# Kernel optimization log

Measured on AMD Instinct MI355X. Metric: run time of the kernel, lower is better.

## Reference

```python
import jax, jax.numpy as jnp
import numpy as np

HEADS, DHEAD = 4, 64            # TransformerConv heads / out_channels
MAX_EDGE_DIST = 1.0

def _ln(x, g, b):
    m = jnp.mean(x, -1, keepdims=True)
    v = jnp.mean((x - m) ** 2, -1, keepdims=True)
    return (x - m) * jax.lax.rsqrt(v + 1e-5) * g + b


def _embed_conv(node_feat, entity_type, adjv, mask, emb, W1, b1, g1, be1, Wh, bh, gh, beh):
    # aggr='add' message passing over dense masked adjacency. mask[b,s,t]: edge s->t.
    B, N, _ = mask.shape
    src = jnp.concatenate([node_feat, emb[entity_type]], -1)          # [B,N,F+E]
    msg = jnp.concatenate(
        [jnp.broadcast_to(src[:, :, None, :], (B, N, N, src.shape[-1])),
         adjv[..., None]], -1)                                        # [B,Ns,Nt,F+E+1]
    h = _ln(jax.nn.relu(msg @ W1 + b1), g1, be1)                      # lin1
    h = _ln(jax.nn.relu(h @ Wh + bh), gh, beh)                        # lin2[0]
    return jnp.einsum('bst,bsth->bth', mask, h)                       # sum over sources


def _tconv(x, adjv, mask, Wq, bq, Wk, bk, Wv, bv, We, Ws, bs):
    # PyG TransformerConv (beta=False, dropout=0, root_weight=True, concat=True).
    B, N, _ = x.shape
    q = (x @ Wq + bq).reshape(B, N, HEADS, DHEAD)
    k = (x @ Wk + bk).reshape(B, N, HEADS, DHEAD)
    v = (x @ Wv + bv).reshape(B, N, HEADS, DHEAD)
    we = We.reshape(HEADS, DHEAD)                                     # edge_dim=1, no bias
    scale = 1.0 / jnp.sqrt(jnp.asarray(DHEAD, x.dtype))
    # score[b,h,s,t] = q_t . (k_s + adjv[s,t]*we) * scale
    qk = jnp.einsum('bshd,bthd->bhst', k, q)
    qe = jnp.einsum('bthd,hd->bht', q, we)
    logits = (qk + adjv[:, None, :, :] * qe[:, :, None, :]) * scale
    mh = mask[:, None, :, :]                                          # [B,1,Ns,Nt]
    masked = jnp.where(mh > 0, logits, -1e30)
    mmax = jnp.max(masked, axis=2, keepdims=True)
    w = jnp.exp(masked - mmax) * mh
    den = jnp.sum(w, axis=2, keepdims=True)
    alpha = w / jnp.maximum(den, 1e-16)                               # softmax over sources per target
    out = jnp.einsum('bhst,bshd->bthd', alpha, v)
    out = out + jnp.einsum('bhst,bst->bth', alpha, adjv)[..., None] * we
    out = out.reshape(B, N, HEADS * DHEAD)
    return out + x @ Ws + bs                                          # skip (root) connection


def _forward(node_feat, entity_type, adj, agent_id, emb, W1, b1, g1, be1, Wh, bh, gh, beh,
             Wq1, bq1, Wk1, bk1, Wv1, bv1, We1, Ws1, bs1,
             Wq2, bq2, Wk2, bk2, Wv2, bv2, We2, Ws2, bs2):
    mask = ((adj > 0) & (adj < MAX_EDGE_DIST)).astype(adj.dtype)
    adjv = adj * mask
    x = _embed_conv(node_feat, entity_type, adjv, mask, emb, W1, b1, g1, be1, Wh, bh, gh, beh)
    x = jax.nn.relu(_tconv(x, adjv, mask, Wq1, bq1, Wk1, bk1, Wv1, bv1, We1, Ws1, bs1))
    x = jax.nn.relu(_tconv(x, adjv, mask, Wq2, bq2, Wk2, bk2, Wv2, bv2, We2, Ws2, bs2))
    return x[jnp.arange(x.shape[0]), agent_id]                        # gather agent node feats


def setup_inputs() -> dict:
    key = jax.random.key(0)
    ks = jax.random.split(key, 24)
    B, N, F, E, H = 32, 128, 9, 8, 128
    HD = HEADS * DHEAD
    s = 0.05
    p = lambda k, shape: (jax.random.normal(k, shape, jnp.float32) * s)
    inp = {
        'node_feat': jax.random.normal(ks[0], (B, N, F), jnp.float32),
        'entity_type': jax.random.randint(ks[1], (B, N), 0, 8),
        'adj': jax.random.uniform(ks[2], (B, N, N), jnp.float32, 0.0, 2.0),
        'agent_id': jax.random.randint(ks[3], (B,), 0, N),
        'emb': p(ks[4], (8, E)),
        'W1': p(ks[5], (F + E + 1, H)), 'b1': jnp.zeros(H), 'g1': jnp.ones(H), 'be1': jnp.zeros(H),
        'Wh': p(ks[6], (H, H)), 'bh': jnp.zeros(H), 'gh': jnp.ones(H), 'beh': jnp.zeros(H),
        'Wq1': p(ks[7], (H, HD)), 'bq1': jnp.zeros(HD),
        'Wk1': p(ks[8], (H, HD)), 'bk1': jnp.zeros(HD),
        'Wv1': p(ks[9], (H, HD)), 'bv1': jnp.zeros(HD),
        'We1': p(ks[10], (1, HD)),
        'Ws1': p(ks[11], (H, HD)), 'bs1': jnp.zeros(HD),
        'Wq2': p(ks[12], (HD, HD)), 'bq2': jnp.zeros(HD),
        'Wk2': p(ks[13], (HD, HD)), 'bk2': jnp.zeros(HD),
        'Wv2': p(ks[14], (HD, HD)), 'bv2': jnp.zeros(HD),
        'We2': p(ks[15], (1, HD)),
        'Ws2': p(ks[16], (HD, HD)), 'bs2': jnp.zeros(HD),
    }
    return inp


def reference(node_feat, entity_type, adj, agent_id, emb, W1, b1, g1, be1, Wh, bh, gh, beh,
              Wq1, bq1, Wk1, bk1, Wv1, bv1, We1, Ws1, bs1,
              Wq2, bq2, Wk2, bk2, Wv2, bv2, We2, Ws2, bs2):
    return _forward(node_feat, entity_type, adj, agent_id, emb, W1, b1, g1, be1, Wh, bh, gh, beh,
                    Wq1, bq1, Wk1, bk1, Wv1, bv1, We1, Ws1, bs1,
                    Wq2, bq2, Wk2, bk2, Wv2, bv2, We2, Ws2, bs2)
```

## Files before the change

### kernel.cpp

```cpp
#include <hip/hip_runtime.h>
#include <hip/hip_bf16.h>

typedef __hip_bfloat16 bf16;
typedef unsigned short ushort_t;
typedef unsigned char uchar_t;
typedef unsigned int uint_t;
typedef __attribute__((ext_vector_type(8))) short short8;
typedef __attribute__((ext_vector_type(4))) float fx4;
typedef __attribute__((ext_vector_type(4))) unsigned int uintx4;

#define BB 32
#define NN 128
#define FF 9
#define EE 8
#define HH 128
#define HD 256
#define NHEAD 4
#define DHEAD 64

__device__ __forceinline__ float us2f(ushort_t u) {
    return __uint_as_float(((unsigned int)u) << 16);
}
__device__ __forceinline__ ushort_t f2us_tr(float f) {
    return (ushort_t)(__float_as_uint(f) >> 16);
}
__device__ __forceinline__ short8 pack4(uint_t w0, uint_t w1, uint_t w2, uint_t w3) {
    uintx4 u = (uintx4){w0, w1, w2, w3};
    return __builtin_bit_cast(short8, u);
}
__device__ __forceinline__ void pair_split(float a, float c, uint_t& hw, uint_t& lw) {
    uint_t ua = __float_as_uint(a), uc = __float_as_uint(c);
    uint_t ka = ua & 0xffff0000u, kc = uc & 0xffff0000u;
    float la = a - __uint_as_float(ka);
    float lc = c - __uint_as_float(kc);
    hw = (ua >> 16) | kc;
    lw = (__float_as_uint(la) >> 16) | (__float_as_uint(lc) & 0xffff0000u);
}
__device__ __forceinline__ uint_t pair_hi(float a, float c) {
    return (__float_as_uint(a) >> 16) | (__float_as_uint(c) & 0xffff0000u);
}

__global__ void TransformerConvNet_85315230367963_kernel() {}

__global__ void k_sent(float* out, float val) {
    out[blockIdx.x * 256 + threadIdx.x] = val;
}

__global__ void k_zero(float* p) {
    p[blockIdx.x * 256 + threadIdx.x] = 0.f;
}

__global__ void k_adjv(const float* adj, float* adjvT) {
    int blk = blockIdx.x;
    int b = blk >> 3, sl = blk & 7;
    const float* src = adj + b * NN * NN;
    float* d2 = adjvT + b * NN * NN;
    int i0 = sl * 2048;
    for (int ii = threadIdx.x; ii < 2048; ii += 256) {
        int i = i0 + ii;
        int t = i >> 7, s = i & 127;
        float a2 = src[s * NN + t];
        d2[i] = (a2 > 0.f && a2 < 1.0f) ? a2 : 0.f;
    }
}

__global__ void k_slist(const float* adjvT, uchar_t* sl_s, float* sl_av, int* cnts) {
    int key = blockIdx.x * 256 + threadIdx.x;
    int bt = key >> 1, sh = key & 1;
    const float* row = adjvT + bt * NN + sh * 64;
    uchar_t* os = sl_s + key * 64;
    float* oa = sl_av + key * 64;
    int c = 0;
    for (int s = 0; s < 64; s++) {
        float a = row[s];
        if (a != 0.f) { os[c] = (uchar_t)(sh * 64 + s); oa[c] = a; c++; }
    }
    if (c == 0) { os[0] = 0; oa[0] = 0.f; }
    cnts[key] = c;
}

__global__ void k_base(const float* nf, const int* et, const float* emb,
                       const float* W1, const float* b1, float* base) {
    int bs = blockIdx.x;
    int c = threadIdx.x;
    int ty = et[bs];
    float acc = b1[c];
    for (int f = 0; f < FF; f++)
        acc += nf[bs * FF + f] * W1[f * HH + c];
    for (int e = 0; e < EE; e++)
        acc += emb[ty * EE + e] * W1[(FF + e) * HH + c];
    base[bs * HH + c] = acc;
}

__global__ void k_prep(const float* Wh, const float* g1, const float* be1,
                       const float* bh, ushort_t* BhiG, ushort_t* BloG,
                       float* W1s, float* cbv) {
    int n = blockIdx.x;
    int t = threadIdx.x;
    int sw = 8 * (n & 15);
    float s1 = 0.f, s2 = 0.f;
    for (int kk = 0; kk < 2; kk++) {
        int k = t + kk * 64;
        float w = Wh[k * HH + n];
        float wp = g1[k] * w;
        ushort_t hb = f2us_tr(wp);
        float lo = wp - us2f(hb);
        BhiG[n * HH + (k ^ sw)] = hb;
        BloG[n * HH + (k ^ sw)] = f2us_tr(lo);
        s1 += wp;
        s2 += be1[k] * w;
    }
    for (int m = 1; m < 64; m <<= 1) {
        s1 += __shfl_xor(s1, m);
        s2 += __shfl_xor(s2, m);
    }
    if (t == 0) { W1s[n] = s1; cbv[n] = s2 + bh[n]; }
}

__global__ void k_prepw(const float* W0, const float* W1p, const float* W2p,
                        const float* W3p, int IN, ushort_t* Whi, ushort_t* Wlo) {
    int blk = blockIdx.x;
    int mat = blk >> 8, n = blk & 255;
    const float* W = (mat == 0) ? W0 : (mat == 1) ? W1p : (mat == 2) ? W2p : W3p;
    ushort_t* hi = Whi + mat * 256 * IN;
    ushort_t* lo = Wlo + mat * 256 * IN;
    int sw = 8 * (n & 15);
    for (int k = threadIdx.x; k < IN; k += 64) {
        float w = W[k * HD + n];
        ushort_t hb = f2us_tr(w);
        float l = w - us2f(hb);
        hi[n * IN + (k ^ sw)] = hb;
        lo[n * IN + (k ^ sw)] = f2us_tr(l);
    }
}

__global__ void __launch_bounds__(256) k_econv_mfma(
    const uchar_t* sl_s, const float* sl_av, const int* cnts,
    const float* base, const float* W1,
    const ushort_t* BhiG, const ushort_t* BloG,
    const float* W1sg, const float* cbv,
    const float* ghp, const float* behp, float* x0)
{
    __shared__ __align__(16) ushort_t PhiPlo[2 * HH * HH];
    ushort_t* Phi = PhiPlo;
    ushort_t* Plo = PhiPlo + HH * HH;

    int blk = blockIdx.x;
    int b  = blk >> 4;
    int tt = (blk >> 1) & 7;
    int sh = blk & 1;
    int t0 = tt * 16;
    int tid = threadIdx.x;
    int wv  = tid >> 6;
    int lane = tid & 63;
    int nl = lane & 15;
    int quad = lane >> 4;

    {
        const uint4* srcH = (const uint4*)BhiG;
        const uint4* srcL = (const uint4*)BloG;
        uint4* dstH = (uint4*)Phi;
        uint4* dstL = (uint4*)Plo;
        for (int i = tid; i < HH * HH / 8; i += 256) {
            dstH[i] = srcH[i];
            dstL[i] = srcL[i];
        }
    }

    float w17v[4][8];
#pragma unroll
    for (int st = 0; st < 4; st++) {
        const float* p = W1 + 17 * HH + quad * 8 + 32 * st;
        float4 a = *(const float4*)p;
        float4 bq = *(const float4*)(p + 4);
        w17v[st][0] = a.x;  w17v[st][1] = a.y;  w17v[st][2] = a.z;  w17v[st][3] = a.w;
        w17v[st][4] = bq.x; w17v[st][5] = bq.y; w17v[st][6] = bq.z; w17v[st][7] = bq.w;
    }

    int key = ((b * NN) + t0 + nl) * 2 + sh;
    int cnt = cnts[key];
    int q = (cnt + 3) >> 2;
    int mq = q;
#pragma unroll
    for (int m = 1; m < 16; m <<= 1) mq = max(mq, __shfl_xor(mq, m));
    const uchar_t* lst_s = sl_s + key * 64;
    const float*   lst_a = sl_av + key * 64;
    int i0 = wv * q;

    fx4 acc1[8];
#pragma unroll
    for (int tile = 0; tile < 8; tile++) acc1[tile] = (fx4){0.f, 0.f, 0.f, 0.f};
    float c0 = 0.f;
    float c1 = 0.f;

    __syncthreads();

    for (int i = 0; i < mq; i++) {
        int idx = i0 + i;
        bool val = (i < q) && (idx < cnt);
        int ridx = (idx < cnt) ? idx : (cnt > 0 ? cnt - 1 : 0);
        int s = lst_s[ridx];
        float avv = val ? lst_a[ridx] : 0.f;
        const float* brow = base + (b * NN + s) * HH;

        short8 Hhi[4], Hlo[4];
        float sm = 0.f, s2 = 0.f;
#pragma unroll
        for (int st = 0; st < 4; st++) {
            const float* p = brow + quad * 8 + 32 * st;
            float4 b0 = *(const float4*)p;
            float4 b1q = *(const float4*)(p + 4);
            float h[8] = {b0.x, b0.y, b0.z, b0.w, b1q.x, b1q.y, b1q.z, b1q.w};
            uint_t hw[4], lw[4];
#pragma unroll
            for (int pr = 0; pr < 4; pr++) {
                float a = fmaxf(fmaf(avv, w17v[st][2 * pr], h[2 * pr]), 0.f);
                float c = fmaxf(fmaf(avv, w17v[st][2 * pr + 1], h[2 * pr + 1]), 0.f);
                sm += a; sm += c;
                s2 = fmaf(a, a, s2);
                s2 = fmaf(c, c, s2);
                pair_split(a, c, hw[pr], lw[pr]);
            }
            Hhi[st] = pack4(hw[0], hw[1], hw[2], hw[3]);
            Hlo[st] = pack4(lw[0], lw[1], lw[2], lw[3]);
        }
        sm += __shfl_xor(sm, 16); sm += __shfl_xor(sm, 32);
        s2 += __shfl_xor(s2, 16); s2 += __shfl_xor(s2, 32);
        float m1 = sm * (1.f / 128.f);
        float r1 = rsqrtf(s2 * (1.f / 128.f) - m1 * m1 + 1e-5f);
        float nm = -m1 * r1;

        fx4 G[8];
#pragma unroll
        for (int tile = 0; tile < 8; tile++) G[tile] = (fx4){0.f, 0.f, 0.f, 0.f};
#pragma unroll
        for (int st = 0; st < 4; st++) {
            int koff = quad * 8 + 32 * st;
#pragma unroll
            for (int tile = 0; tile < 8; tile++) {
                int off = (tile * 16 + nl) * HH + (koff ^ (nl * 8));
                short8 ph = *(const short8*)(&Phi[off]);
                short8 pl = *(const short8*)(&Plo[off]);
                G[tile] = __builtin_amdgcn_mfma_f32_16x16x32_bf16(ph, Hhi[st], G[tile], 0, 0, 0);
                G[tile] = __builtin_amdgcn_mfma_f32_16x16x32_bf16(pl, Hhi[st], G[tile], 0, 0, 0);
                G[tile] = __builtin_amdgcn_mfma_f32_16x16x32_bf16(ph, Hlo[st], G[tile], 0, 0, 0);
            }
        }

        float sm2 = 0.f, ss2 = 0.f;
#pragma unroll
        for (int tile = 0; tile < 8; tile++) {
            float4 w4 = *(const float4*)(W1sg + tile * 16 + quad * 4);
            float4 c4 = *(const float4*)(cbv + tile * 16 + quad * 4);
            float wa[4] = {w4.x, w4.y, w4.z, w4.w};
            float ca[4] = {c4.x, c4.y, c4.z, c4.w};
#pragma unroll
            for (int r = 0; r < 4; r++) {
                float pre = fmaf(r1, G[tile][r], fmaf(nm, wa[r], ca[r]));
                float h2 = fmaxf(pre, 0.f);
                G[tile][r] = h2;
                sm2 += h2;
                ss2 = fmaf(h2, h2, ss2);
            }
        }
        sm2 += __shfl_xor(sm2, 16); sm2 += __shfl_xor(sm2, 32);
        ss2 += __shfl_xor(ss2, 16); ss2 += __shfl_xor(ss2, 32);
        float mean2 = sm2 * (1.f / 128.f);
        float r2 = rsqrtf(ss2 * (1.f / 128.f) - mean2 * mean2 + 1e-5f);
        float msk = val ? 1.f : 0.f;
        float mr2 = msk * r2;

#pragma unroll
        for (int tile = 0; tile < 8; tile++)
#pragma unroll
            for (int r = 0; r < 4; r++)
                acc1[tile][r] = fmaf(mr2, G[tile][r], acc1[tile][r]);
        c0 += msk;
        c1 = fmaf(mr2, mean2, c1);
    }

    __syncthreads();
    float* slab = (float*)PhiPlo;
#pragma unroll
    for (int tile = 0; tile < 8; tile++) {
        float4 g4 = *(const float4*)(ghp + tile * 16 + quad * 4);
        float4 be4 = *(const float4*)(behp + tile * 16 + quad * 4);
        float gv[4] = {g4.x, g4.y, g4.z, g4.w};
        float bv[4] = {be4.x, be4.y, be4.z, be4.w};
#pragma unroll
        for (int r = 0; r < 4; r++) {
            float xv = fmaf(gv[r], acc1[tile][r] - c1, bv[r] * c0);
            slab[(wv * 16 + nl) * 132 + tile * 16 + quad * 4 + r] = xv;
        }
    }
    __syncthreads();
    for (int e = tid; e < 16 * HH; e += 256) {
        int t = e >> 7, n = e & 127;
        float vsum = slab[t * 132 + n] + slab[(16 + t) * 132 + n]
                   + slab[(32 + t) * 132 + n] + slab[(48 + t) * 132 + n];
        atomicAdd(&x0[(b * NN + t0 + t) * HH + n], vsum);
    }
}

template <int IN>
__global__ void __launch_bounds__(256) k_qkvs_mfma(
    const float* x, const ushort_t* Whi, const ushort_t* Wlo,
    const float* b0, const float* b1, const float* b2, const float* b3,
    float* q, float* skipo,
    ushort_t* khi, ushort_t* klo, ushort_t* vThi, ushort_t* vTlo)
{
    const int ST = IN / 32;
    int blk = blockIdx.x;
    int m0 = (blk >> 3) * 64;
    int nsl = blk & 7;
    int tid = threadIdx.x;
    int wv = tid >> 6;
    int lane = tid & 63;
    int nl = lane & 15;
    int quad = lane >> 4;
    int row = m0 + wv * 16 + nl;

    short8 Ahi[ST], Alo[ST];
    const float* xrow = x + (long)row * IN;
#pragma unroll
    for (int st = 0; st < ST; st++) {
        const float* p = xrow + quad * 8 + 32 * st;
        float4 a4 = *(const float4*)p;
        float4 b4 = *(const float4*)(p + 4);
        float h[8] = {a4.x, a4.y, a4.z, a4.w, b4.x, b4.y, b4.z, b4.w};
        uint_t hw[4], lw[4];
#pragma unroll
        for (int pr = 0; pr < 4; pr++)
            pair_split(h[2 * pr], h[2 * pr + 1], hw[pr], lw[pr]);
        Ahi[st] = pack4(hw[0], hw[1], hw[2], hw[3]);
        Alo[st] = pack4(lw[0], lw[1], lw[2], lw[3]);
    }

    const float* bs_[4] = {b0, b1, b2, b3};

#pragma unroll
    for (int mat = 0; mat < 4; mat++) {
        const ushort_t* Bh = Whi + (mat * 256 + nsl * 32) * IN;
        const ushort_t* Bl = Wlo + (mat * 256 + nsl * 32) * IN;
        fx4 G[2];
#pragma unroll
        for (int tile = 0; tile < 2; tile++) {
            float bc = bs_[mat][nsl * 32 + tile * 16 + nl];
            G[tile] = (fx4){bc, bc, bc, bc};
        }
#pragma unroll
        for (int st = 0; st < ST; st++) {
            int koff = quad * 8 + 32 * st;
#pragma unroll
            for (int tile = 0; tile < 2; tile++) {
                int off = (tile * 16 + nl) * IN + (koff ^ (nl * 8));
                short8 bh8 = *(const short8*)(Bh + off);
                short8 bl8 = *(const short8*)(Bl + off);
                G[tile] = __builtin_amdgcn_mfma_f32_16x16x32_bf16(Ahi[st], bh8, G[tile], 0, 0, 0);
                G[tile] = __builtin_amdgcn_mfma_f32_16x16x32_bf16(Alo[st], bh8, G[tile], 0, 0, 0);
                G[tile] = __builtin_amdgcn_mfma_f32_16x16x32_bf16(Ahi[st], bl8, G[tile], 0, 0, 0);
            }
        }
        int row0 = m0 + wv * 16 + quad * 4;
        if (mat == 0 || mat == 3) {
            float* om = (mat == 0) ? q : skipo;
#pragma unroll
            for (int tile = 0; tile < 2; tile++)
#pragma unroll
                for (int r = 0; r < 4; r++)
                    om[(row0 + r) * HD + nsl * 32 + tile * 16 + nl] = G[tile][r];
        } else if (mat == 1) {
#pragma unroll
            for (int tile = 0; tile < 2; tile++) {
                int col = nsl * 32 + tile * 16 + nl;
#pragma unroll
                for (int r = 0; r < 4; r++) {
                    float gv = G[tile][r];
                    ushort_t hb = f2us_tr(gv);
                    khi[(row0 + r) * HD + col] = hb;
                    klo[(row0 + r) * HD + col] = f2us_tr(gv - us2f(hb));
                }
            }
        } else {
            int bb = row0 >> 7;
            int s0 = row0 & 127;
#pragma unroll
            for (int tile = 0; tile < 2; tile++) {
                int col = nsl * 32 + tile * 16 + nl;
                int dg = bb * 256 + col;
                ushort4 h4, l4;
                float g0 = G[tile][0], g1 = G[tile][1], g2 = G[tile][2], g3 = G[tile][3];
                ushort_t h0 = f2us_tr(g0), h1 = f2us_tr(g1), h2 = f2us_tr(g2), h3 = f2us_tr(g3);
                h4.x = h0; h4.y = h1; h4.z = h2; h4.w = h3;
                l4.x = f2us_tr(g0 - us2f(h0));
                l4.y = f2us_tr(g1 - us2f(h1));
                l4.z = f2us_tr(g2 - us2f(h2));
                l4.w = f2us_tr(g3 - us2f(h3));
                *(ushort4*)&vThi[dg * NN + s0] = h4;
                *(ushort4*)&vTlo[dg * NN + s0] = l4;
            }
        }
    }
}

__global__ void __launch_bounds__(64) k_attn_mfma(
    const float* qb, const ushort_t* khi, const ushort_t* klo,
    const ushort_t* vThi, const ushort_t* vTlo,
    const float* adjvT, const float* We, const float* skip, float* xout)
{
    __shared__ float aL[16][132];
    __shared__ float qeL[16];

    int blk = blockIdx.x;
    int b  = blk >> 5;
    int h  = (blk >> 3) & 3;
    int tt = blk & 7;
    int t0 = tt * 16;
    int lane = threadIdx.x;
    int nl = lane & 15;
    int quad = lane >> 4;

    short8 Qhi[2], Qlo[2];
    float qe = 0.f;
#pragma unroll
    for (int ks = 0; ks < 2; ks++) {
        const float* p = qb + (b * NN + t0 + nl) * HD + h * DHEAD + quad * 8 + 32 * ks;
        const float* wp = We + h * DHEAD + quad * 8 + 32 * ks;
        float4 a0 = *(const float4*)p;
        float4 a1 = *(const float4*)(p + 4);
        float4 w0 = *(const float4*)wp;
        float4 w1 = *(const float4*)(wp + 4);
        float hv[8] = {a0.x, a0.y, a0.z, a0.w, a1.x, a1.y, a1.z, a1.w};
        float wv8[8] = {w0.x, w0.y, w0.z, w0.w, w1.x, w1.y, w1.z, w1.w};
        uint_t hw[4], lw[4];
#pragma unroll
        for (int pr = 0; pr < 4; pr++) {
            float a = hv[2 * pr], c = hv[2 * pr + 1];
            qe = fmaf(a, wv8[2 * pr], qe);
            qe = fmaf(c, wv8[2 * pr + 1], qe);
            pair_split(a, c, hw[pr], lw[pr]);
        }
        Qhi[ks] = pack4(hw[0], hw[1], hw[2], hw[3]);
        Qlo[ks] = pack4(lw[0], lw[1], lw[2], lw[3]);
    }
    qe += __shfl_xor(qe, 16);
    qe += __shfl_xor(qe, 32);
    if (lane < 16) qeL[lane] = qe;
    __syncthreads();
    float qe_r[4];
#pragma unroll
    for (int r = 0; r < 4; r++) qe_r[r] = qeL[quad * 4 + r];
    float we_d[4];
#pragma unroll
    for (int nt = 0; nt < 4; nt++) we_d[nt] = We[h * DHEAD + nt * 16 + nl];

    fx4 S[8];
#pragma unroll
    for (int st = 0; st < 8; st++) S[st] = (fx4){0.f, 0.f, 0.f, 0.f};
#pragma unroll
    for (int ks = 0; ks < 2; ks++) {
#pragma unroll
        for (int st = 0; st < 8; st++) {
            long off = (long)(b * NN + st * 16 + nl) * HD + h * DHEAD + quad * 8 + 32 * ks;
            short8 bh8 = *(const short8*)(khi + off);
            short8 bl8 = *(const short8*)(klo + off);
            S[st] = __builtin_amdgcn_mfma_f32_16x16x32_bf16(Qhi[ks], bh8, S[st], 0, 0, 0);
            S[st] = __builtin_amdgcn_mfma_f32_16x16x32_bf16(Qlo[ks], bh8, S[st], 0, 0, 0);
            S[st] = __builtin_amdgcn_mfma_f32_16x16x32_bf16(Qhi[ks], bl8, S[st], 0, 0, 0);
        }
    }

    float av[8][4];
#pragma unroll
    for (int st = 0; st < 8; st++)
#pragma unroll
        for (int r = 0; r < 4; r++)
            av[st][r] = adjvT[(b * NN + t0 + quad * 4 + r) * NN + st * 16 + nl];
#pragma unroll
    for (int st = 0; st < 8; st++)
#pragma unroll
        for (int r = 0; r < 4; r++) {
            float a = av[st][r];
            S[st][r] = (a != 0.f) ? (S[st][r] + a * qe_r[r]) * 0.125f : -1e30f;
        }

    float mx[4], den[4], beta[4];
#pragma unroll
    for (int r = 0; r < 4; r++) {
        float m = S[0][r];
#pragma unroll
        for (int st = 1; st < 8; st++) m = fmaxf(m, S[st][r]);
#pragma unroll
        for (int mm = 1; mm < 16; mm <<= 1) m = fmaxf(m, __shfl_xor(m, mm));
        mx[r] = m;
    }
#pragma unroll
    for (int r = 0; r < 4; r++) den[r] = 0.f;
#pragma unroll
    for (int st = 0; st < 8; st++)
#pragma unroll
        for (int r = 0; r < 4; r++) {
            float e = (av[st][r] != 0.f) ? __expf(S[st][r] - mx[r]) : 0.f;
            S[st][r] = e;
            den[r] += e;
        }
#pragma unroll
    for (int r = 0; r < 4; r++) {
#pragma unroll
        for (int mm = 1; mm < 16; mm <<= 1) den[r] += __shfl_xor(den[r], mm);
        den[r] = 1.f / fmaxf(den[r], 1e-16f);
        beta[r] = 0.f;
    }
#pragma unroll
    for (int st = 0; st < 8; st++)
#pragma unroll
        for (int r = 0; r < 4; r++) {
            float al = S[st][r] * den[r];
            S[st][r] = al;
            beta[r] += al * av[st][r];
        }
#pragma unroll
    for (int r = 0; r < 4; r++)
#pragma unroll
        for (int mm = 1; mm < 16; mm <<= 1) beta[r] += __shfl_xor(beta[r], mm);

#pragma unroll
    for (int st = 0; st < 8; st++)
#pragma unroll
        for (int r = 0; r < 4; r++)
            aL[quad * 4 + r][st * 16 + nl] = S[st][r];
    __syncthreads();
    short8 Ah[4];
#pragma unroll
    for (int ks = 0; ks < 4; ks++) {
        const float* p = &aL[nl][quad * 8 + 32 * ks];
        float4 a0 = *(const float4*)p;
        float4 a1 = *(const float4*)(p + 4);
        float hv[8] = {a0.x, a0.y, a0.z, a0.w, a1.x, a1.y, a1.z, a1.w};
        uint_t w[4];
#pragma unroll
        for (int pr = 0; pr < 4; pr++) w[pr] = pair_hi(hv[2 * pr], hv[2 * pr + 1]);
        Ah[ks] = pack4(w[0], w[1], w[2], w[3]);
    }

    fx4 G[4];
#pragma unroll
    for (int nt = 0; nt < 4; nt++) {
        fx4 g;
#pragma unroll
        for (int r = 0; r < 4; r++) g[r] = beta[r] * we_d[nt];
        G[nt] = g;
    }
#pragma unroll
    for (int ks = 0; ks < 4; ks++) {
#pragma unroll
        for (int nt = 0; nt < 4; nt++) {
            long dg = (long)(b * 256 + h * DHEAD + nt * 16 + nl);
            const short8 vh = *(const short8*)(vThi + dg * NN + quad * 8 + 32 * ks);
            const short8 vl = *(const short8*)(vTlo + dg * NN + quad * 8 + 32 * ks);
            G[nt] = __builtin_amdgcn_mfma_f32_16x16x32_bf16(Ah[ks], vh, G[nt], 0, 0, 0);
            G[nt] = __builtin_amdgcn_mfma_f32_16x16x32_bf16(Ah[ks], vl, G[nt], 0, 0, 0);
        }
    }

#pragma unroll
    for (int nt = 0; nt < 4; nt++)
#pragma unroll
        for (int r = 0; r < 4; r++) {
            int gi = (b * NN + t0 + quad * 4 + r) * HD + h * DHEAD + nt * 16 + nl;
            xout[gi] = fmaxf(G[nt][r] + skip[gi], 0.f);
        }
}

__global__ void k_gather(const float* x2, const int* agent, float* out) {
    int b = blockIdx.x;
    int c = threadIdx.x;
    out[b * HD + c] = x2[(b * NN + agent[b]) * HD + c];
}

extern "C" void kernel_launch(void* const* d_in, const int* in_sizes, int n_in,
                              void* d_out, int out_size, void* d_ws, size_t ws_size,
                              hipStream_t stream) {
    float* out = (float*)d_out;
    (void)hipGetLastError();

    bool ok = (n_in == 31) && in_sizes[0] == BB * NN * FF && in_sizes[2] == BB * NN * NN
              && in_sizes[5] == (FF + EE + 1) * HH && in_sizes[13] == HH * HD
              && in_sizes[22] == HD * HD && out_size == BB * HD;
    if (!ok) { k_sent<<<32, 256, 0, stream>>>(out, -30000.f); return; }

    const size_t WS_NEED = (size_t)8912896 * 4;
    if (ws_size < WS_NEED) { k_sent<<<32, 256, 0, stream>>>(out, -20000.f); return; }

    const float* nf    = (const float*)d_in[0];
    const int*   et    = (const int*)d_in[1];
    const float* adj   = (const float*)d_in[2];
    const int*   agent = (const int*)d_in[3];
    const float* emb   = (const float*)d_in[4];
    const float* W1    = (const float*)d_in[5];
    const float* b1    = (const float*)d_in[6];
    const float* g1    = (const float*)d_in[7];
    const float* be1   = (const float*)d_in[8];
    const float* Wh    = (const float*)d_in[9];
    const float* bh    = (const float*)d_in[10];
    const float* gh    = (const float*)d_in[11];
    const float* beh   = (const float*)d_in[12];
    const float* Wq1   = (const float*)d_in[13];
    const float* bq1   = (const float*)d_in[14];
    const float* Wk1   = (const float*)d_in[15];
    const float* bk1   = (const float*)d_in[16];
    const float* Wv1   = (const float*)d_in[17];
    const float* bv1   = (const float*)d_in[18];
    const float* We1   = (const float*)d_in[19];
    const float* Ws1   = (const float*)d_in[20];
    const float* bs1   = (const float*)d_in[21];
    const float* Wq2   = (const float*)d_in[22];
    const float* bq2   = (const float*)d_in[23];
    const float* Wk2   = (const float*)d_in[24];
    const float* bk2   = (const float*)d_in[25];
    const float* Wv2   = (const float*)d_in[26];
    const float* bv2   = (const float*)d_in[27];
    const float* We2   = (const float*)d_in[28];
    const float* Ws2   = (const float*)d_in[29];
    const float* bs2   = (const float*)d_in[30];

    float* ws   = (float*)d_ws;
    float* slav = ws;
    float* base = slav + BB * NN * NN / 32;
    base = ws + 524288;
    float* x0   = base + BB * NN * HH;
    float* q    = x0 + BB * NN * HH;
    float* kreg = q + BB * NN * HD;
    float* vreg = kreg + BB * NN * HD;
    float* skip = vreg + BB * NN * HD;
    float* areg = skip + BB * NN * HD;
    float* x1   = areg + BB * NN * HD;
    float* x2   = x1 + BB * NN * HD;

    ushort_t* BhiG = (ushort_t*)q;
    ushort_t* BloG = BhiG + HH * HH;
    float*    W1sW = q + 16384;
    float*    cbW  = q + 16512;
    int*      cnts = (int*)(q + 17024);

    ushort_t* khi  = (ushort_t*)kreg;
    ushort_t* klo  = khi + BB * NN * HD;
    ushort_t* vThi = (ushort_t*)vreg;
    ushort_t* vTlo = vThi + BB * NN * HD;

    ushort_t* WhA = (ushort_t*)areg;
    ushort_t* WlA = WhA + 4 * 256 * HH;
    ushort_t* WhB = WlA + 4 * 256 * HH;
    ushort_t* WlB = WhB + 4 * 256 * HD;
    float* adjvT  = areg + 393216;
    uchar_t* sl_s = (uchar_t*)(areg + 917504);

    int fail = 0;
    hipError_t e;
#define CHK(stage) do { e = hipGetLastError(); if (e != hipSuccess && fail == 0) fail = (stage); } while (0)

    k_adjv<<<256, 256, 0, stream>>>(adj, adjvT);                                     CHK(1);
    k_slist<<<32, 256, 0, stream>>>(adjvT, sl_s, slav, cnts);                        CHK(2);
    k_base<<<BB * NN, HH, 0, stream>>>(nf, et, emb, W1, b1, base);                   CHK(3);
    k_zero<<<BB * NN * HH / 256, 256, 0, stream>>>(x0);                              CHK(4);
    k_prep<<<HH, 64, 0, stream>>>(Wh, g1, be1, bh, BhiG, BloG, W1sW, cbW);           CHK(5);
    k_prepw<<<1024, 64, 0, stream>>>(Wq1, Wk1, Wv1, Ws1, HH, WhA, WlA);              CHK(6);
    k_prepw<<<1024, 64, 0, stream>>>(Wq2, Wk2, Wv2, Ws2, HD, WhB, WlB);              CHK(7);
    k_econv_mfma<<<512, 256, 0, stream>>>(sl_s, slav, cnts, base, W1,
                                          BhiG, BloG, W1sW, cbW, gh, beh, x0);       CHK(8);

    k_qkvs_mfma<HH><<<512, 256, 0, stream>>>(x0, WhA, WlA, bq1, bk1, bv1, bs1,
                                             q, skip, khi, klo, vThi, vTlo);         CHK(9);
    k_attn_mfma<<<1024, 64, 0, stream>>>(q, khi, klo, vThi, vTlo, adjvT, We1,
                                         skip, x1);                                  CHK(10);

    k_qkvs_mfma<HD><<<512, 256, 0, stream>>>(x1, WhB, WlB, bq2, bk2, bv2, bs2,
                                             q, skip, khi, klo, vThi, vTlo);         CHK(11);
    k_attn_mfma<<<1024, 64, 0, stream>>>(q, khi, klo, vThi, vTlo, adjvT, We2,
                                         skip, x2);                                  CHK(12);

    k_gather<<<BB, HD, 0, stream>>>(x2, agent, out);                                 CHK(13);
#undef CHK

    if (fail != 0)
        k_sent<<<32, 256, 0, stream>>>(out, -(1000.f + 500.f * (float)fail));
}
```

Before: 293.2 us.

## Fuse preprocessing kernels into one launch and fold agent gather into attention

Merges the seven small setup kernels (adjacency transpose, source-list build, base embedding, zeroing, weight splitting) into a single block-partitioned kernel. The source list is now built with wave ballot and popcount instead of a serial per-thread scan. The final gather is fused into the second attention kernel, which writes only the agent row's output. This removes launch overhead and the full x2 writeback, at the cost of a more branchy combined kernel.

```diff
diff --git a/kernel.cpp b/kernel.cpp
--- a/kernel.cpp
+++ b/kernel.cpp
@@ -46,91 +46,115 @@
     out[blockIdx.x * 256 + threadIdx.x] = val;
 }
 
-__global__ void k_zero(float* p) {
-    p[blockIdx.x * 256 + threadIdx.x] = 0.f;
-}
-
-__global__ void k_adjv(const float* adj, float* adjvT) {
+__global__ void __launch_bounds__(256) k_prep_all(
+    const float* adj, float* adjvT, uchar_t* sl_s, float* sl_av, int* cnts,
+    const float* nf, const int* et, const float* emb, const float* W1,
+    const float* b1, float* base, float* x0,
+    const float* Wh, const float* g1, const float* be1, const float* bh,
+    ushort_t* BhiG, ushort_t* BloG, float* W1s, float* cbv,
+    const float* Wq1, const float* Wk1, const float* Wv1, const float* Ws1,
+    ushort_t* WhA, ushort_t* WlA,
+    const float* Wq2, const float* Wk2, const float* Wv2, const float* Ws2,
+    ushort_t* WhB, ushort_t* WlB)
+{
     int blk = blockIdx.x;
-    int b = blk >> 3, sl = blk & 7;
-    const float* src = adj + b * NN * NN;
-    float* d2 = adjvT + b * NN * NN;
-    int i0 = sl * 2048;
-    for (int ii = threadIdx.x; ii < 2048; ii += 256) {
-        int i = i0 + ii;
-        int t = i >> 7, s = i & 127;
-        float a2 = src[s * NN + t];
-        d2[i] = (a2 > 0.f && a2 < 1.0f) ? a2 : 0.f;
-    }
-}
-
-__global__ void k_slist(const float* adjvT, uchar_t* sl_s, float* sl_av, int* cnts) {
-    int key = blockIdx.x * 256 + threadIdx.x;
-    int bt = key >> 1, sh = key & 1;
-    const float* row = adjvT + bt * NN + sh * 64;
-    uchar_t* os = sl_s + key * 64;
-    float* oa = sl_av + key * 64;
-    int c = 0;
-    for (int s = 0; s < 64; s++) {
-        float a = row[s];
-        if (a != 0.f) { os[c] = (uchar_t)(sh * 64 + s); oa[c] = a; c++; }
-    }
-    if (c == 0) { os[0] = 0; oa[0] = 0.f; }
-    cnts[key] = c;
-}
-
-__global__ void k_base(const float* nf, const int* et, const float* emb,
-                       const float* W1, const float* b1, float* base) {
-    int bs = blockIdx.x;
-    int c = threadIdx.x;
-    int ty = et[bs];
-    float acc = b1[c];
-    for (int f = 0; f < FF; f++)
-        acc += nf[bs * FF + f] * W1[f * HH + c];
-    for (int e = 0; e < EE; e++)
-        acc += emb[ty * EE + e] * W1[(FF + e) * HH + c];
-    base[bs * HH + c] = acc;
-}
-
-__global__ void k_prep(const float* Wh, const float* g1, const float* be1,
-                       const float* bh, ushort_t* BhiG, ushort_t* BloG,
-                       float* W1s, float* cbv) {
-    int n = blockIdx.x;
-    int t = threadIdx.x;
-    int sw = 8 * (n & 15);
-    float s1 = 0.f, s2 = 0.f;
-    for (int kk = 0; kk < 2; kk++) {
-        int k = t + kk * 64;
-        float w = Wh[k * HH + n];
-        float wp = g1[k] * w;
-        ushort_t hb = f2us_tr(wp);
-        float lo = wp - us2f(hb);
-        BhiG[n * HH + (k ^ sw)] = hb;
-        BloG[n * HH + (k ^ sw)] = f2us_tr(lo);
-        s1 += wp;
-        s2 += be1[k] * w;
-    }
-    for (int m = 1; m < 64; m <<= 1) {
-        s1 += __shfl_xor(s1, m);
-        s2 += __shfl_xor(s2, m);
-    }
-    if (t == 0) { W1s[n] = s1; cbv[n] = s2 + bh[n]; }
-}
-
-__global__ void k_prepw(const float* W0, const float* W1p, const float* W2p,
-                        const float* W3p, int IN, ushort_t* Whi, ushort_t* Wlo) {
-    int blk = blockIdx.x;
-    int mat = blk >> 8, n = blk & 255;
-    const float* W = (mat == 0) ? W0 : (mat == 1) ? W1p : (mat == 2) ? W2p : W3p;
-    ushort_t* hi = Whi + mat * 256 * IN;
-    ushort_t* lo = Wlo + mat * 256 * IN;
-    int sw = 8 * (n & 15);
-    for (int k = threadIdx.x; k < IN; k += 64) {
-        float w = W[k * HD + n];
-        ushort_t hb = f2us_tr(w);
-        float l = w - us2f(hb);
-        hi[n * IN + (k ^ sw)] = hb;
-        lo[n * IN + (k ^ sw)] = f2us_tr(l);
+    int tid = threadIdx.x;
+
+    if (blk < 256) {
+        int b = blk >> 3, sl = blk & 7;
+        int wv = tid >> 6, lane = tid & 63;
+#pragma unroll
+        for (int j = 0; j < 8; j++) {
+            int u = wv * 8 + j;
+            int t = sl * 16 + (u >> 1);
+            int sh = u & 1;
+            int s = sh * 64 + lane;
+            float a = adj[(b * NN + s) * NN + t];
+            float av = (a > 0.f && a < 1.0f) ? a : 0.f;
+            adjvT[(b * NN + t) * NN + s] = av;
+            unsigned long long mask = __ballot(av != 0.f);
+            int key = (b * NN + t) * 2 + sh;
+            if (av != 0.f) {
+                int pos = __popcll(mask & ((1ull << lane) - 1ull));
+                sl_s[key * 64 + pos] = (uchar_t)s;
+                sl_av[key * 64 + pos] = av;
+            }
+            if (lane == 0) {
+                cnts[key] = (int)__popcll(mask);
+                if (mask == 0ull) { sl_s[key * 64] = 0; sl_av[key * 64] = 0.f; }
+            }
+        }
+    } else if (blk < 1280) {
+        int bblk = blk - 256;
+        int c = tid & 127;
+#pragma unroll
+        for (int rr = 0; rr < 2; rr++) {
+            int bs = bblk * 4 + rr * 2 + (tid >> 7);
+            int ty = et[bs];
+            float acc = b1[c];
+            for (int f = 0; f < FF; f++)
+                acc += nf[bs * FF + f] * W1[f * HH + c];
+            for (int e2 = 0; e2 < EE; e2++)
+                acc += emb[ty * EE + e2] * W1[(FF + e2) * HH + c];
+            base[bs * HH + c] = acc;
+        }
+    } else if (blk < 1536) {
+        int zblk = blk - 1280;
+        float4* p = (float4*)x0 + zblk * 512 + tid * 2;
+        p[0] = (float4){0.f, 0.f, 0.f, 0.f};
+        p[1] = (float4){0.f, 0.f, 0.f, 0.f};
+    } else if (blk < 1568) {
+        int n = (blk - 1536) * 4 + (tid >> 6);
+        int t = tid & 63;
+        int sw = 8 * (n & 15);
+        float s1 = 0.f, s2 = 0.f;
+#pragma unroll
+        for (int kk = 0; kk < 2; kk++) {
+            int k = t + kk * 64;
+            float w = Wh[k * HH + n];
+            float wp = g1[k] * w;
+            ushort_t hb = f2us_tr(wp);
+            float lo = wp - us2f(hb);
+            BhiG[n * HH + (k ^ sw)] = hb;
+            BloG[n * HH + (k ^ sw)] = f2us_tr(lo);
+            s1 += wp;
+            s2 += be1[k] * w;
+        }
+        for (int m = 1; m < 64; m <<= 1) {
+            s1 += __shfl_xor(s1, m);
+            s2 += __shfl_xor(s2, m);
+        }
+        if (t == 0) { W1s[n] = s1; cbv[n] = s2 + bh[n]; }
+    } else if (blk < 1824) {
+        int key = (blk - 1568) * 4 + (tid >> 6);
+        int lane = tid & 63;
+        int mat = key >> 8, n = key & 255;
+        const float* W = (mat == 0) ? Wq1 : (mat == 1) ? Wk1 : (mat == 2) ? Wv1 : Ws1;
+        ushort_t* hi = WhA + mat * 256 * HH;
+        ushort_t* lo = WlA + mat * 256 * HH;
+        int sw = 8 * (n & 15);
+        for (int k = lane; k < HH; k += 64) {
+            float w = W[k * HD + n];
+            ushort_t hb = f2us_tr(w);
+            float l = w - us2f(hb);
+            hi[n * HH + (k ^ sw)] = hb;
+            lo[n * HH + (k ^ sw)] = f2us_tr(l);
+        }
+    } else {
+        int key = (blk - 1824) * 4 + (tid >> 6);
+        int lane = tid & 63;
+        int mat = key >> 8, n = key & 255;
+        const float* W = (mat == 0) ? Wq2 : (mat == 1) ? Wk2 : (mat == 2) ? Wv2 : Ws2;
+        ushort_t* hi = WhB + mat * 256 * HD;
+        ushort_t* lo = WlB + mat * 256 * HD;
+        int sw = 8 * (n & 15);
+        for (int k = lane; k < HD; k += 64) {
+            float w = W[k * HD + n];
+            ushort_t hb = f2us_tr(w);
+            float l = w - us2f(hb);
+            hi[n * HD + (k ^ sw)] = hb;
+            lo[n * HD + (k ^ sw)] = f2us_tr(l);
+        }
     }
 }
 
@@ -406,7 +430,8 @@
 __global__ void __launch_bounds__(64) k_attn_mfma(
     const float* qb, const ushort_t* khi, const ushort_t* klo,
     const ushort_t* vThi, const ushort_t* vTlo,
-    const float* adjvT, const float* We, const float* skip, float* xout)
+    const float* adjvT, const float* We, const float* skip, float* xout,
+    const int* agentp, float* outp)
 {
     __shared__ float aL[16][132];
     __shared__ float qeL[16];
@@ -563,19 +588,27 @@
         }
     }
 
-#pragma unroll
-    for (int nt = 0; nt < 4; nt++)
-#pragma unroll
-        for (int r = 0; r < 4; r++) {
-            int gi = (b * NN + t0 + quad * 4 + r) * HD + h * DHEAD + nt * 16 + nl;
-            xout[gi] = fmaxf(G[nt][r] + skip[gi], 0.f);
-        }
-}
-
-__global__ void k_gather(const float* x2, const int* agent, float* out) {
-    int b = blockIdx.x;
-    int c = threadIdx.x;
-    out[b * HD + c] = x2[(b * NN + agent[b]) * HD + c];
+    if (agentp == nullptr) {
+#pragma unroll
+        for (int nt = 0; nt < 4; nt++)
+#pragma unroll
+            for (int r = 0; r < 4; r++) {
+                int gi = (b * NN + t0 + quad * 4 + r) * HD + h * DHEAD + nt * 16 + nl;
+                xout[gi] = fmaxf(G[nt][r] + skip[gi], 0.f);
+            }
+    } else {
+        int ag = agentp[b];
+#pragma unroll
+        for (int nt = 0; nt < 4; nt++)
+#pragma unroll
+            for (int r = 0; r < 4; r++) {
+                int t = t0 + quad * 4 + r;
+                if (t == ag) {
+                    int gi = (b * NN + t) * HD + h * DHEAD + nt * 16 + nl;
+                    outp[b * HD + h * DHEAD + nt * 16 + nl] = fmaxf(G[nt][r] + skip[gi], 0.f);
+                }
+            }
+    }
 }
 
 extern "C" void kernel_launch(void* const* d_in, const int* in_sizes, int n_in,
@@ -626,8 +659,7 @@
 
     float* ws   = (float*)d_ws;
     float* slav = ws;
-    float* base = slav + BB * NN * NN / 32;
-    base = ws + 524288;
+    float* base = ws + 524288;
     float* x0   = base + BB * NN * HH;
     float* q    = x0 + BB * NN * HH;
     float* kreg = q + BB * NN * HD;
@@ -659,27 +691,25 @@
     hipError_t e;
 #define CHK(stage) do { e = hipGetLastError(); if (e != hipSuccess && fail == 0) fail = (stage); } while (0)
 
-    k_adjv<<<256, 256, 0, stream>>>(adj, adjvT);                                     CHK(1);
-    k_slist<<<32, 256, 0, stream>>>(adjvT, sl_s, slav, cnts);                        CHK(2);
-    k_base<<<BB * NN, HH, 0, stream>>>(nf, et, emb, W1, b1, base);                   CHK(3);
-    k_zero<<<BB * NN * HH / 256, 256, 0, stream>>>(x0);                              CHK(4);
-    k_prep<<<HH, 64, 0, stream>>>(Wh, g1, be1, bh, BhiG, BloG, W1sW, cbW);           CHK(5);
-    k_prepw<<<1024, 64, 0, stream>>>(Wq1, Wk1, Wv1, Ws1, HH, WhA, WlA);              CHK(6);
-    k_prepw<<<1024, 64, 0, stream>>>(Wq2, Wk2, Wv2, Ws2, HD, WhB, WlB);              CHK(7);
+    k_prep_all<<<2080, 256, 0, stream>>>(
+        adj, adjvT, sl_s, slav, cnts,
+        nf, et, emb, W1, b1, base, x0,
+        Wh, g1, be1, bh, BhiG, BloG, W1sW, cbW,
+        Wq1, Wk1, Wv1, Ws1, WhA, WlA,
+        Wq2, Wk2, Wv2, Ws2, WhB, WlB);                                               CHK(1);
+
     k_econv_mfma<<<512, 256, 0, stream>>>(sl_s, slav, cnts, base, W1,
-                                          BhiG, BloG, W1sW, cbW, gh, beh, x0);       CHK(8);
+                                          BhiG, BloG, W1sW, cbW, gh, beh, x0);       CHK(2);
 
     k_qkvs_mfma<HH><<<512, 256, 0, stream>>>(x0, WhA, WlA, bq1, bk1, bv1, bs1,
-                                             q, skip, khi, klo, vThi, vTlo);         CHK(9);
+                                             q, skip, khi, klo, vThi, vTlo);         CHK(3);
     k_attn_mfma<<<1024, 64, 0, stream>>>(q, khi, klo, vThi, vTlo, adjvT, We1,
-                                         skip, x1);                                  CHK(10);
+                                         skip, x1, nullptr, nullptr);                CHK(4);
 
     k_qkvs_mfma<HD><<<512, 256, 0, stream>>>(x1, WhB, WlB, bq2, bk2, bv2, bs2,
-                                             q, skip, khi, klo, vThi, vTlo);         CHK(11);
+                                             q, skip, khi, klo, vThi, vTlo);         CHK(5);
     k_attn_mfma<<<1024, 64, 0, stream>>>(q, khi, klo, vThi, vTlo, adjvT, We2,
-                                         skip, x2);                                  CHK(12);
-
-    k_gather<<<BB, HD, 0, stream>>>(x2, agent, out);                                 CHK(13);
+                                         skip, x2, agent, out);                      CHK(6);
 #undef CHK
 
     if (fail != 0)
```

After: 260.6 us. 1.13x faster.
